# Optimization experiments

Hardware: AMD Instinct MI355X
Metric: run time of the kernel (lower is better)

## Reference

```python
import jax, jax.numpy as jnp
import numpy as np

N, L, V, IN_DIM, H, E = 128, 128, 8000, 64, 13, 2048
G = 4 * H  # LSTM gate dim (52)

def _lstm_scan(xs, Wih, Whh, b, h0, c0):
    # xs: [L, N, D]; returns final (h, c), each [N, H]
    def step(carry, x_t):
        h, c = carry
        g = x_t @ Wih.T + h @ Whh.T + b
        i, f, gg, o = jnp.split(g, 4, axis=-1)
        c = jax.nn.sigmoid(f) * c + jax.nn.sigmoid(i) * jnp.tanh(gg)
        h = jax.nn.sigmoid(o) * jnp.tanh(c)
        return (h, c), None
    (h, c), _ = jax.lax.scan(step, (h0, c0), xs)
    return h, c

def _gcn_layer(x, W, b, src, dst, norm):
    # GCNConv: out[t] = sum_{(s,t)} norm_st * (x W)[s] + b  (self loops included in src/dst)
    msg = (x @ W)[src] * norm[:, None]
    return jax.ops.segment_sum(msg, dst, num_segments=N) + b

def _gnn(x, params, src, dst, norm):
    W1, b1, W2, b2, Wf, bf = params
    x = jax.nn.leaky_relu(_gcn_layer(x, W1, b1, src, dst, norm), 0.01)
    x = jax.nn.leaky_relu(_gcn_layer(x, W2, b2, src, dst, norm), 0.01)
    return x @ Wf + bf

def setup_inputs():
    ks = iter(jax.random.split(jax.random.key(0), 64))
    def rn(*shape):
        return jax.random.normal(next(ks), shape, dtype=jnp.float32) * 0.1
    inp = {}
    inp["x_tokens"] = jax.random.randint(next(ks), (N, L), 0, V, dtype=jnp.int32)
    inp["edge_index"] = jax.random.randint(next(ks), (2, E), 0, N, dtype=jnp.int32)
    inp["emb"] = rn(V + 1, IN_DIM).at[V].set(0.0)  # padding_idx row zeroed
    for d in ("f", "b"):
        inp["Wih_%s_enc" % d] = rn(G, IN_DIM)
        inp["Whh_%s_enc" % d] = rn(G, H)
        inp["b_%s_enc" % d] = rn(G)
    inp["Wp1"] = rn(2 * H, 2 * H); inp["bp1"] = rn(2 * H)
    inp["Wp2"] = rn(2 * H, 2 * H); inp["bp2"] = rn(2 * H)
    for g in ("gh", "gc"):
        inp[g + "_W1"] = rn(2 * H, 16); inp[g + "_b1"] = rn(16)
        inp[g + "_W2"] = rn(16, 32);    inp[g + "_b2"] = rn(32)
        inp[g + "_Wf"] = rn(32, 2 * H); inp[g + "_bf"] = rn(2 * H)
    for d in ("f", "b"):
        inp["Wih_%s_dec" % d] = rn(G, 1)
        inp["Whh_%s_dec" % d] = rn(G, H)
        inp["b_%s_dec" % d] = rn(G)
    inp["Wout"] = rn(V, 2 * H); inp["bout"] = rn(V)
    return inp

def reference(x_tokens, edge_index, emb, Wih_f_enc, Whh_f_enc, b_f_enc, Wih_b_enc, Whh_b_enc, b_b_enc, Wp1, bp1, Wp2, bp2, gh_W1, gh_b1, gh_W2, gh_b2, gh_Wf, gh_bf, gc_W1, gc_b1, gc_W2, gc_b2, gc_Wf, gc_bf, Wih_f_dec, Whh_f_dec, b_f_dec, Wih_b_dec, Whh_b_dec, b_b_dec, Wout, bout):
    # --- per-node biLSTM encode ---
    xs = jnp.swapaxes(emb[x_tokens], 0, 1)          # [L, N, IN_DIM]
    z = jnp.zeros((N, H), jnp.float32)
    hf, cf = _lstm_scan(xs, Wih_f_enc, Whh_f_enc, b_f_enc, z, z)
    hb, cb = _lstm_scan(xs[::-1], Wih_b_enc, Whh_b_enc, b_b_enc, z, z)
    state_h = jnp.concatenate([hf, hb], -1) @ Wp1.T + bp1   # [N, 2H]
    state_c = jnp.concatenate([cf, cb], -1) @ Wp2.T + bp2
    # --- GCN fusion (symmetric norm with self loops) ---
    ar = jnp.arange(N, dtype=edge_index.dtype)
    src = jnp.concatenate([edge_index[0], ar])
    dst = jnp.concatenate([edge_index[1], ar])
    deg = jax.ops.segment_sum(jnp.ones_like(src, jnp.float32), dst, num_segments=N)
    dinv = jax.lax.rsqrt(jnp.maximum(deg, 1.0))
    norm = dinv[src] * dinv[dst]
    sh = _gnn(state_h, (gh_W1, gh_b1, gh_W2, gh_b2, gh_Wf, gh_bf), src, dst, norm).reshape(N, 2, H)
    sc = _gnn(state_c, (gc_W1, gc_b1, gc_W2, gc_b2, gc_Wf, gc_bf), src, dst, norm).reshape(N, 2, H)
    # --- decoder: each step is a single-timestep biLSTM; original code only
    # passes the GNN state at step 0 and uses a fresh ZERO state for i>0 ---
    prev = jnp.concatenate([jnp.full((N, 1), -1.0, jnp.float32), x_tokens[:, :-1].astype(jnp.float32)], axis=1)  # [N, L]
    first = (jnp.arange(L) == 0)[None, :, None]
    def dec_cell(h0, c0, Wih, Whh, b):
        g = prev[..., None] * Wih[:, 0] + jnp.einsum('nlh,gh->nlg', h0, Whh) + b
        i, f, gg, o = jnp.split(g, 4, axis=-1)
        c = jax.nn.sigmoid(f) * c0 + jax.nn.sigmoid(i) * jnp.tanh(gg)
        return jax.nn.sigmoid(o) * jnp.tanh(c)
    h_f = dec_cell(jnp.where(first, sh[:, 0][:, None, :], 0.0), jnp.where(first, sc[:, 0][:, None, :], 0.0), Wih_f_dec, Whh_f_dec, b_f_dec)
    h_b = dec_cell(jnp.where(first, sh[:, 1][:, None, :], 0.0), jnp.where(first, sc[:, 1][:, None, :], 0.0), Wih_b_dec, Whh_b_dec, b_b_dec)
    dec_out = jnp.concatenate([h_f, h_b], -1)       # [N, L, 2H]
    return jnp.einsum('nld,vd->nlv', dec_out, Wout) + bout   # [N, L, V]
```

## Files before the change

kernel.cpp:

```cpp
#include <hip/hip_runtime.h>
#include <stdint.h>

#define N_    128
#define L_    128
#define V_    8000
#define IN_   64
#define H_    13
#define G_    52
#define E_    2048
#define TWOH  26
#define TOTW  742808

typedef unsigned int   u32;
typedef unsigned short u16;

__device__ __forceinline__ float bfu(u16 u){
    u32 x = ((u32)u) << 16; float f; __builtin_memcpy(&f, &x, 4); return f;
}
__device__ __forceinline__ float sigf(float x){
    x = fminf(fmaxf(x, -30.f), 30.f);
    return 1.0f / (1.0f + __expf(-x));
}
__device__ __forceinline__ float tanh_(float x){
    x = fminf(fmaxf(x, -15.f), 15.f);
    float e = __expf(2.0f * x); return 1.0f - 2.0f / (e + 1.0f);
}

__global__ __launch_bounds__(64) void k_detect(const u16* __restrict__ emb_u16,
                                               int* __restrict__ flag){
    const int lane = threadIdx.x;
    int wild = 0;
    for (int i = lane; i < 1024; i += 64){
        u16 u = emb_u16[i];
        int e = (u >> 7) & 0xFF;
        int tame = (u == 0) || (u == 0x8000) || (e >= 0x60 && e <= 0x88);
        wild += !tame;
    }
    #pragma unroll
    for (int o = 32; o; o >>= 1) wild += __shfl_down(wild, o, 64);
    if (lane == 0) *flag = (wild > 200) ? 1 : 0;
}

struct P31 { const void* p[31]; };

__global__ __launch_bounds__(256) void k_convert(P31 a, const int* __restrict__ flag,
                                                 float* __restrict__ cw){
    const int fp32 = *flag;
    const int i = blockIdx.x * 256 + threadIdx.x;
    if (i >= TOTW) return;
    const int offs[32] = {
        0, 512064, 515392, 516068, 516120, 519448, 520124, 520176, 520852,
        520878, 521554, 521580, 521996, 522012, 522524, 522556, 523388,
        523414, 523830, 523846, 524358, 524390, 525222, 525248, 525300,
        525976, 526028, 526080, 526756, 526808, 734808, TOTW };
    int seg = 0;
    while (i >= offs[seg + 1]) ++seg;
    const int k = i - offs[seg];
    cw[i] = fp32 ? ((const float*)a.p[seg])[k] : bfu(((const u16*)a.p[seg])[k]);
}

__global__ __launch_bounds__(128) void k_proj(const float* __restrict__ emb,
                                              const float* __restrict__ WihF,
                                              const float* __restrict__ WihB,
                                              float* __restrict__ projF,
                                              float* __restrict__ projB){
    __shared__ float x[IN_];
    const int t = blockIdx.x;
    const int tid = threadIdx.x;
    if (tid < IN_) x[tid] = emb[t * IN_ + tid];
    __syncthreads();
    if (tid < 2 * G_){
        const int dir = tid / G_;
        const int g   = tid - dir * G_;
        const float* w = (dir ? WihB : WihF) + g * IN_;
        float acc = 0.f;
        #pragma unroll
        for (int i = 0; i < IN_; ++i) acc += x[i] * w[i];
        (dir ? projB : projF)[t * G_ + g] = acc;
    }
}

__global__ __launch_bounds__(128) void k_lstm(const int* __restrict__ toks_g,
        const float* __restrict__ projF, const float* __restrict__ projB,
        const float* __restrict__ WhhF, const float* __restrict__ bF,
        const float* __restrict__ WhhB, const float* __restrict__ bB,
        const float* __restrict__ Wp1, const float* __restrict__ bp1,
        const float* __restrict__ Wp2, const float* __restrict__ bp2,
        float* __restrict__ state_h, float* __restrict__ state_c){
    __shared__ int   toks[L_];
    __shared__ float hcat[TWOH];
    __shared__ float ccat[TWOH];
    const int n = blockIdx.x, tid = threadIdx.x;
    const int wave = tid >> 6, lane = tid & 63;
    if (tid < L_) toks[tid] = toks_g[n * L_ + tid];

    const float* proj = wave ? projB : projF;
    const float* Whh  = wave ? WhhB : WhhF;
    const float* bp   = wave ? bB   : bF;

    float wh[H_];
    #pragma unroll
    for (int j = 0; j < H_; ++j) wh[j] = 0.f;
    float bb = 0.f;
    if (lane < G_){
        bb = bp[lane];
        #pragma unroll
        for (int j = 0; j < H_; ++j) wh[j] = Whh[lane * H_ + j];
    }
    __syncthreads();

    float h = 0.f, c = 0.f;
    int tok0 = wave ? toks[L_ - 1] : toks[0];
    float gpre = (lane < G_) ? proj[tok0 * G_ + lane] : 0.f;

    for (int t = 0; t < L_; ++t){
        float gv = gpre + bb;
        if (t + 1 < L_){
            int tn = wave ? toks[L_ - 2 - t] : toks[t + 1];
            gpre = (lane < G_) ? proj[tn * G_ + lane] : 0.f;
        }
        #pragma unroll
        for (int j = 0; j < H_; ++j) gv += __shfl(h, j, 64) * wh[j];
        float iv = __shfl(gv, lane,      64);
        float fv = __shfl(gv, lane + 13, 64);
        float gg = __shfl(gv, lane + 26, 64);
        float ov = __shfl(gv, lane + 39, 64);
        c = sigf(fv) * c + sigf(iv) * tanh_(gg);
        h = sigf(ov) * tanh_(c);
    }

    if (lane < H_){ hcat[wave * H_ + lane] = h; ccat[wave * H_ + lane] = c; }
    __syncthreads();

    if (lane < TWOH){
        if (wave == 0){
            float a = bp1[lane];
            #pragma unroll
            for (int k = 0; k < TWOH; ++k) a += hcat[k] * Wp1[lane * TWOH + k];
            state_h[n * TWOH + lane] = a;
        } else {
            float a = bp2[lane];
            #pragma unroll
            for (int k = 0; k < TWOH; ++k) a += ccat[k] * Wp2[lane * TWOH + k];
            state_c[n * TWOH + lane] = a;
        }
    }
}

__global__ __launch_bounds__(256) void k_gcn(const int* __restrict__ eidx,
        const float* __restrict__ state_h, const float* __restrict__ state_c,
        const float* gh_W1, const float* gh_b1, const float* gh_W2, const float* gh_b2,
        const float* gh_Wf, const float* gh_bf,
        const float* gc_W1, const float* gc_b1, const float* gc_W2, const float* gc_b2,
        const float* gc_Wf, const float* gc_bf,
        float* __restrict__ sh, float* __restrict__ sc){
    __shared__ float xs[N_][33];
    __shared__ float dinv[N_];
    __shared__ float xw[N_][32];
    __shared__ float acc[N_][32];
    const int tid = threadIdx.x;
    const int p = blockIdx.x;
    const float* xin = p ? state_c : state_h;
    const float* W1  = p ? gc_W1 : gh_W1;  const float* b1  = p ? gc_b1 : gh_b1;
    const float* W2  = p ? gc_W2 : gh_W2;  const float* b2  = p ? gc_b2 : gh_b2;
    const float* Wf  = p ? gc_Wf : gh_Wf;  const float* bfp = p ? gc_bf : gh_bf;
    float* outp = p ? sc : sh;

    for (int i = tid; i < N_ * TWOH; i += 256) xs[i / TWOH][i % TWOH] = xin[i];
    for (int i = tid; i < N_; i += 256) dinv[i] = 1.0f;
    __syncthreads();
    for (int e = tid; e < E_; e += 256) atomicAdd(&dinv[eidx[E_ + e]], 1.0f);
    __syncthreads();
    for (int i = tid; i < N_; i += 256) dinv[i] = rsqrtf(dinv[i]);
    __syncthreads();

    for (int i = tid; i < N_ * 16; i += 256){
        int nn = i >> 4, f = i & 15;
        float a = 0.f;
        #pragma unroll
        for (int k = 0; k < TWOH; ++k) a += xs[nn][k] * W1[k * 16 + f];
        xw[nn][f] = a;
    }
    __syncthreads();
    for (int i = tid; i < N_ * 16; i += 256){ int nn = i >> 4, f = i & 15; acc[nn][f] = dinv[nn] * dinv[nn] * xw[nn][f]; }
    __syncthreads();
    for (int e = tid; e < E_; e += 256){
        int s = eidx[e], d = eidx[E_ + e];
        float nm = dinv[s] * dinv[d];
        #pragma unroll
        for (int f = 0; f < 16; ++f) atomicAdd(&acc[d][f], nm * xw[s][f]);
    }
    __syncthreads();
    for (int i = tid; i < N_ * 16; i += 256){
        int nn = i >> 4, f = i & 15;
        float a = acc[nn][f] + b1[f];
        xs[nn][f] = a > 0.f ? a : 0.01f * a;
    }
    __syncthreads();

    for (int i = tid; i < N_ * 32; i += 256){
        int nn = i >> 5, f = i & 31;
        float a = 0.f;
        #pragma unroll
        for (int k = 0; k < 16; ++k) a += xs[nn][k] * W2[k * 32 + f];
        xw[nn][f] = a;
    }
    __syncthreads();
    for (int i = tid; i < N_ * 32; i += 256){ int nn = i >> 5, f = i & 31; acc[nn][f] = dinv[nn] * dinv[nn] * xw[nn][f]; }
    __syncthreads();
    for (int e = tid; e < E_; e += 256){
        int s = eidx[e], d = eidx[E_ + e];
        float nm = dinv[s] * dinv[d];
        #pragma unroll
        for (int f = 0; f < 32; ++f) atomicAdd(&acc[d][f], nm * xw[s][f]);
    }
    __syncthreads();
    for (int i = tid; i < N_ * 32; i += 256){
        int nn = i >> 5, f = i & 31;
        float a = acc[nn][f] + b2[f];
        xs[nn][f] = a > 0.f ? a : 0.01f * a;
    }
    __syncthreads();

    for (int i = tid; i < N_ * TWOH; i += 256){
        int nn = i / TWOH, d = i % TWOH;
        float a = bfp[d];
        #pragma unroll
        for (int k = 0; k < 32; ++k) a += xs[nn][k] * Wf[k * TWOH + d];
        outp[i] = a;
    }
}

__global__ __launch_bounds__(256) void k_dec(const int* __restrict__ toks,
        const float* __restrict__ sh, const float* __restrict__ sc,
        const float* WihF, const float* WhhF, const float* bF,
        const float* WihB, const float* WhhB, const float* bB,
        float* __restrict__ dec){
    __shared__ float wih[2][G_], bias[2][G_], whh[2][G_][H_];
    const int tid = threadIdx.x;
    for (int i = tid; i < 2 * G_; i += 256){
        int d = i / G_, k = i % G_;
        wih[d][k]  = (d ? WihB : WihF)[k];
        bias[d][k] = (d ? bB : bF)[k];
    }
    for (int i = tid; i < 2 * G_ * H_; i += 256){
        int d = i / (G_ * H_), rr = i % (G_ * H_), k = rr / H_, j = rr % H_;
        whh[d][k][j] = (d ? WhhB : WhhF)[k * H_ + j];
    }
    __syncthreads();

    const int r = blockIdx.x * 256 + tid;
    const int n = r >> 7, l = r & 127;
    const bool first = (l == 0);
    const float prev = first ? -1.0f : (float)toks[n * L_ + l - 1];

    for (int d = 0; d < 2; ++d){
        float h0[H_], c0[H_];
        #pragma unroll
        for (int j = 0; j < H_; ++j){
            h0[j] = first ? sh[n * TWOH + d * H_ + j] : 0.f;
            c0[j] = first ? sc[n * TWOH + d * H_ + j] : 0.f;
        }
        #pragma unroll
        for (int j = 0; j < H_; ++j){
            float gi = prev * wih[d][j]      + bias[d][j];
            float gf = prev * wih[d][13 + j] + bias[d][13 + j];
            float gg = prev * wih[d][26 + j] + bias[d][26 + j];
            float go = prev * wih[d][39 + j] + bias[d][39 + j];
            if (first){
                #pragma unroll
                for (int k = 0; k < H_; ++k){
                    float hk = h0[k];
                    gi += hk * whh[d][j][k];
                    gf += hk * whh[d][13 + j][k];
                    gg += hk * whh[d][26 + j][k];
                    go += hk * whh[d][39 + j][k];
                }
            }
            float cc = sigf(gf) * c0[j] + sigf(gi) * tanh_(gg);
            float hh = sigf(go) * tanh_(cc);
            dec[(size_t)r * TWOH + d * H_ + j] = hh;
        }
    }
}

#define RT 64
#define VT 512
__global__ __launch_bounds__(256) void k_out(const float* __restrict__ dec,
        const float* __restrict__ Wout, const float* __restrict__ bout,
        float* __restrict__ out){
    __shared__ float dl[RT * 28];
    __shared__ float wl[VT * 26];
    const int tid = threadIdx.x;
    const int r0 = blockIdx.x * RT;
    const int v0 = blockIdx.y * VT;
    const int nv = min(VT, V_ - v0);

    for (int i = tid; i < RT * 28; i += 256){
        int rr = i / 28, k = i % 28;
        dl[i] = (k < TWOH) ? dec[(size_t)(r0 + rr) * TWOH + k] : 0.f;
    }
    {
        const float4* src = (const float4*)(Wout + (size_t)v0 * TWOH);
        float4* dst = (float4*)wl;
        const int n4 = nv * TWOH / 4;
        for (int i = tid; i < n4; i += 256) dst[i] = src[i];
    }
    __syncthreads();

    const int lv = 2 * tid;
    if (lv < nv){
        float wa[28], wb[28];
        #pragma unroll
        for (int k = 0; k < TWOH; ++k){ wa[k] = wl[lv * TWOH + k]; wb[k] = wl[(lv + 1) * TWOH + k]; }
        wa[26] = wa[27] = wb[26] = wb[27] = 0.f;
        const int v = v0 + lv;
        const float ba = bout[v], bb2 = bout[v + 1];
        float2* outp = (float2*)(out + (size_t)r0 * V_ + v);
        for (int rr = 0; rr < RT; ++rr){
            const float* dp = dl + rr * 28;
            float sA = ba, sB = bb2;
            #pragma unroll
            for (int k = 0; k < 28; ++k){ float dk = dp[k]; sA += dk * wa[k]; sB += dk * wb[k]; }
            outp[(size_t)rr * (V_ / 2)] = make_float2(sA, sB);
        }
    }
}

extern "C" void kernel_launch(void* const* d_in, const int* in_sizes, int n_in,
                              void* d_out, int out_size, void* d_ws, size_t ws_size,
                              hipStream_t stream){
    int*   flag  = (int*)d_ws;
    float* cw    = (float*)d_ws + 64;
    float* projF = cw + TOTW;
    float* projB = projF + 416000;
    float* state_h = projB + 416000;
    float* state_c = state_h + 3328;
    float* sh      = state_c + 3328;
    float* sc      = sh + 3328;
    float* dec     = sc + 3328;

    float* cEmb   = cw + 0;
    float* cWihF  = cw + 512064;
    float* cWhhF  = cw + 515392;
    float* cbF    = cw + 516068;
    float* cWihB  = cw + 516120;
    float* cWhhB  = cw + 519448;
    float* cbB    = cw + 520124;
    float* cWp1   = cw + 520176;
    float* cbp1   = cw + 520852;
    float* cWp2   = cw + 520878;
    float* cbp2   = cw + 521554;
    float* cghW1  = cw + 521580;
    float* cghb1  = cw + 521996;
    float* cghW2  = cw + 522012;
    float* cghb2  = cw + 522524;
    float* cghWf  = cw + 522556;
    float* cghbf  = cw + 523388;
    float* cgcW1  = cw + 523414;
    float* cgcb1  = cw + 523830;
    float* cgcW2  = cw + 523846;
    float* cgcb2  = cw + 524358;
    float* cgcWf  = cw + 524390;
    float* cgcbf  = cw + 525222;
    float* cWihFd = cw + 525248;
    float* cWhhFd = cw + 525300;
    float* cbFd   = cw + 525976;
    float* cWihBd = cw + 526028;
    float* cWhhBd = cw + 526080;
    float* cbBd   = cw + 526756;
    float* cWout  = cw + 526808;
    float* cbout  = cw + 734808;

    const int* x_tokens   = (const int*)d_in[0];
    const int* edge_index = (const int*)d_in[1];

    P31 a;
    for (int j = 0; j < 31; ++j) a.p[j] = d_in[2 + j];

    k_detect<<<1, 64, 0, stream>>>((const u16*)d_in[2], flag);
    k_convert<<<(TOTW + 255) / 256, 256, 0, stream>>>(a, flag, cw);
    k_proj<<<V_, 128, 0, stream>>>(cEmb, cWihF, cWihB, projF, projB);
    k_lstm<<<N_, 128, 0, stream>>>(x_tokens, projF, projB,
                                   cWhhF, cbF, cWhhB, cbB,
                                   cWp1, cbp1, cWp2, cbp2, state_h, state_c);
    k_gcn<<<2, 256, 0, stream>>>(edge_index, state_h, state_c,
                                 cghW1, cghb1, cghW2, cghb2, cghWf, cghbf,
                                 cgcW1, cgcb1, cgcW2, cgcb2, cgcWf, cgcbf,
                                 sh, sc);
    k_dec<<<(N_ * L_) / 256, 256, 0, stream>>>(x_tokens, sh, sc,
                                               cWihFd, cWhhFd, cbFd,
                                               cWihBd, cWhhBd, cbBd, dec);
    k_out<<<dim3((N_ * L_) / RT, (V_ + VT - 1) / VT), 256, 0, stream>>>(dec, cWout, cbout, (float*)d_out);
}
```

Baseline: 951.3 us.

## Build CSR in GCN kernel and widen output GEMM to four columns per thread

The GCN kernel now builds a CSR adjacency in shared memory (count, prefix scan, fill) and aggregates by destination with a per-node gather loop, replacing the per-feature shared-memory atomic scatter. Separately, the output projection kernel drops to 128 threads, each computing four vocabulary columns with float4 loads of the decoded row and float4 stores, to raise register reuse and store width. The output kernel writes the large [N,L,V] tensor and dominates runtime. Its change is the main lever, at the cost of higher register pressure and fewer threads per block.

Result: faster. 908.7 us (-4.5%).

```diff
diff --git a/kernel.cpp b/kernel.cpp
--- a/kernel.cpp
+++ b/kernel.cpp
@@ -155,9 +155,12 @@
         const float* gc_Wf, const float* gc_bf,
         float* __restrict__ sh, float* __restrict__ sc){
     __shared__ float xs[N_][33];
+    __shared__ float xw[N_][33];
     __shared__ float dinv[N_];
-    __shared__ float xw[N_][32];
-    __shared__ float acc[N_][32];
+    __shared__ int   ptr[N_ + 1];
+    __shared__ int   cnt[N_];
+    __shared__ int   scn[N_];
+    __shared__ int   srcs[E_];
     const int tid = threadIdx.x;
     const int p = blockIdx.x;
     const float* xin = p ? state_c : state_h;
@@ -167,11 +170,33 @@
     float* outp = p ? sc : sh;
 
     for (int i = tid; i < N_ * TWOH; i += 256) xs[i / TWOH][i % TWOH] = xin[i];
-    for (int i = tid; i < N_; i += 256) dinv[i] = 1.0f;
-    __syncthreads();
-    for (int e = tid; e < E_; e += 256) atomicAdd(&dinv[eidx[E_ + e]], 1.0f);
-    __syncthreads();
-    for (int i = tid; i < N_; i += 256) dinv[i] = rsqrtf(dinv[i]);
+    if (tid < N_) cnt[tid] = 0;
+    __syncthreads();
+    for (int e = tid; e < E_; e += 256) atomicAdd(&cnt[eidx[E_ + e]], 1);
+    __syncthreads();
+    if (tid < N_){
+        dinv[tid] = rsqrtf((float)cnt[tid] + 1.0f);
+        scn[tid]  = cnt[tid];
+    }
+    __syncthreads();
+    for (int off = 1; off < N_; off <<= 1){
+        int v = 0;
+        if (tid < N_ && tid >= off) v = scn[tid - off];
+        __syncthreads();
+        if (tid < N_) scn[tid] += v;
+        __syncthreads();
+    }
+    if (tid < N_){
+        ptr[tid + 1] = scn[tid];
+        if (tid == 0) ptr[0] = 0;
+        cnt[tid] = 0;
+    }
+    __syncthreads();
+    for (int e = tid; e < E_; e += 256){
+        int d = eidx[E_ + e];
+        int pos = atomicAdd(&cnt[d], 1);
+        srcs[ptr[d] + pos] = eidx[e];
+    }
     __syncthreads();
 
     for (int i = tid; i < N_ * 16; i += 256){
@@ -182,18 +207,16 @@
         xw[nn][f] = a;
     }
     __syncthreads();
-    for (int i = tid; i < N_ * 16; i += 256){ int nn = i >> 4, f = i & 15; acc[nn][f] = dinv[nn] * dinv[nn] * xw[nn][f]; }
-    __syncthreads();
-    for (int e = tid; e < E_; e += 256){
-        int s = eidx[e], d = eidx[E_ + e];
-        float nm = dinv[s] * dinv[d];
-        #pragma unroll
-        for (int f = 0; f < 16; ++f) atomicAdd(&acc[d][f], nm * xw[s][f]);
-    }
-    __syncthreads();
     for (int i = tid; i < N_ * 16; i += 256){
         int nn = i >> 4, f = i & 15;
-        float a = acc[nn][f] + b1[f];
+        float dn = dinv[nn];
+        float a = dn * dn * xw[nn][f];
+        const int e1 = ptr[nn + 1];
+        for (int e = ptr[nn]; e < e1; ++e){
+            int s = srcs[e];
+            a += dn * dinv[s] * xw[s][f];
+        }
+        a += b1[f];
         xs[nn][f] = a > 0.f ? a : 0.01f * a;
     }
     __syncthreads();
@@ -206,18 +229,16 @@
         xw[nn][f] = a;
     }
     __syncthreads();
-    for (int i = tid; i < N_ * 32; i += 256){ int nn = i >> 5, f = i & 31; acc[nn][f] = dinv[nn] * dinv[nn] * xw[nn][f]; }
-    __syncthreads();
-    for (int e = tid; e < E_; e += 256){
-        int s = eidx[e], d = eidx[E_ + e];
-        float nm = dinv[s] * dinv[d];
-        #pragma unroll
-        for (int f = 0; f < 32; ++f) atomicAdd(&acc[d][f], nm * xw[s][f]);
-    }
-    __syncthreads();
     for (int i = tid; i < N_ * 32; i += 256){
         int nn = i >> 5, f = i & 31;
-        float a = acc[nn][f] + b2[f];
+        float dn = dinv[nn];
+        float a = dn * dn * xw[nn][f];
+        const int e1 = ptr[nn + 1];
+        for (int e = ptr[nn]; e < e1; ++e){
+            int s = srcs[e];
+            a += dn * dinv[s] * xw[s][f];
+        }
+        a += b2[f];
         xs[nn][f] = a > 0.f ? a : 0.01f * a;
     }
     __syncthreads();
@@ -286,7 +307,7 @@
 
 #define RT 64
 #define VT 512
-__global__ __launch_bounds__(256) void k_out(const float* __restrict__ dec,
+__global__ __launch_bounds__(128) void k_out(const float* __restrict__ dec,
         const float* __restrict__ Wout, const float* __restrict__ bout,
         float* __restrict__ out){
     __shared__ float dl[RT * 28];
@@ -296,33 +317,46 @@
     const int v0 = blockIdx.y * VT;
     const int nv = min(VT, V_ - v0);
 
-    for (int i = tid; i < RT * 28; i += 256){
+    for (int i = tid; i < RT * 28; i += 128){
         int rr = i / 28, k = i % 28;
         dl[i] = (k < TWOH) ? dec[(size_t)(r0 + rr) * TWOH + k] : 0.f;
     }
     {
         const float4* src = (const float4*)(Wout + (size_t)v0 * TWOH);
-        float4* dst = (float4*)wl;
+        float4* dst4 = (float4*)wl;
         const int n4 = nv * TWOH / 4;
-        for (int i = tid; i < n4; i += 256) dst[i] = src[i];
-    }
-    __syncthreads();
-
-    const int lv = 2 * tid;
+        for (int i = tid; i < n4; i += 128) dst4[i] = src[i];
+    }
+    __syncthreads();
+
+    const int lv = 4 * tid;
     if (lv < nv){
-        float wa[28], wb[28];
-        #pragma unroll
-        for (int k = 0; k < TWOH; ++k){ wa[k] = wl[lv * TWOH + k]; wb[k] = wl[(lv + 1) * TWOH + k]; }
-        wa[26] = wa[27] = wb[26] = wb[27] = 0.f;
+        float w[4][28];
+        #pragma unroll
+        for (int c = 0; c < 4; ++c){
+            #pragma unroll
+            for (int k = 0; k < TWOH; ++k) w[c][k] = wl[(lv + c) * TWOH + k];
+            w[c][26] = 0.f; w[c][27] = 0.f;
+        }
         const int v = v0 + lv;
-        const float ba = bout[v], bb2 = bout[v + 1];
-        float2* outp = (float2*)(out + (size_t)r0 * V_ + v);
+        const float b0 = bout[v],     b1 = bout[v + 1];
+        const float b2 = bout[v + 2], b3 = bout[v + 3];
+        float4* outp = (float4*)(out + (size_t)r0 * V_ + v);
+        #pragma unroll 2
         for (int rr = 0; rr < RT; ++rr){
-            const float* dp = dl + rr * 28;
-            float sA = ba, sB = bb2;
+            float4 d4[7];
+            const float4* dp4 = (const float4*)(dl + rr * 28);
             #pragma unroll
-            for (int k = 0; k < 28; ++k){ float dk = dp[k]; sA += dk * wa[k]; sB += dk * wb[k]; }
-            outp[(size_t)rr * (V_ / 2)] = make_float2(sA, sB);
+            for (int j = 0; j < 7; ++j) d4[j] = dp4[j];
+            float s0 = b0, s1 = b1, s2 = b2, s3 = b3;
+            const float* dk = (const float*)d4;
+            #pragma unroll
+            for (int k = 0; k < 28; ++k){
+                float dv = dk[k];
+                s0 += dv * w[0][k]; s1 += dv * w[1][k];
+                s2 += dv * w[2][k]; s3 += dv * w[3][k];
+            }
+            outp[(size_t)rr * (V_ / 4)] = make_float4(s0, s1, s2, s3);
         }
     }
 }
@@ -391,5 +425,5 @@
     k_dec<<<(N_ * L_) / 256, 256, 0, stream>>>(x_tokens, sh, sc,
                                                cWihFd, cWhhFd, cbFd,
                                                cWihBd, cWhhBd, cbBd, dec);
-    k_out<<<dim3((N_ * L_) / RT, (V_ + VT - 1) / VT), 256, 0, stream>>>(dec, cWout, cbout, (float*)d_out);
-}
+    k_out<<<dim3((N_ * L_) / RT, (V_ + VT - 1) / VT), 128, 0, stream>>>(dec, cWout, cbout, (float*)d_out);
+}
```
